# Kernel tuning notes

Hardware: AMD Instinct MI355X
Metric: run time of the kernel (lower is better)

The kernel has to match this reference:

```python
import jax, jax.numpy as jnp
import numpy as np
import math

N_COARSE, N_FINE = 8192, 32768
DEC_DIM, ENC_DIM, OUT_DIM, K = 256, 128, 128, 16
LN_EPS = 1e-5


def setup_inputs() -> dict:
    key = jax.random.key(0)
    ks = jax.random.split(key, 16)
    s = lambda fan_in: 1.0 / math.sqrt(fan_in)
    return {
        "decoder_features": jax.random.normal(ks[0], (N_COARSE, DEC_DIM), jnp.float32),
        "decoder_pos": jax.random.normal(ks[1], (N_COARSE, 3), jnp.float32),
        "encoder_features": jax.random.normal(ks[2], (N_FINE, ENC_DIM), jnp.float32),
        "encoder_pos": jax.random.normal(ks[3], (N_FINE, 3), jnp.float32),
        "encoder_labels": jax.random.randint(ks[4], (N_FINE,), 0, 13, jnp.int64),
        # params (torch nn.Linear default init scale)
        "Wq": jax.random.uniform(ks[5], (DEC_DIM, ENC_DIM), jnp.float32, -s(ENC_DIM), s(ENC_DIM)),
        "bq": jnp.zeros((DEC_DIM,), jnp.float32),
        "Wk": jax.random.uniform(ks[6], (DEC_DIM, DEC_DIM), jnp.float32, -s(DEC_DIM), s(DEC_DIM)),
        "bk": jnp.zeros((DEC_DIM,), jnp.float32),
        "Wv": jax.random.uniform(ks[7], (DEC_DIM, DEC_DIM), jnp.float32, -s(DEC_DIM), s(DEC_DIM)),
        "bv": jnp.zeros((DEC_DIM,), jnp.float32),
        "W1": jax.random.uniform(ks[8], (OUT_DIM, DEC_DIM + ENC_DIM), jnp.float32, -s(DEC_DIM + ENC_DIM), s(DEC_DIM + ENC_DIM)),
        "b1": jnp.zeros((OUT_DIM,), jnp.float32),
        "W2": jax.random.uniform(ks[9], (OUT_DIM, OUT_DIM), jnp.float32, -s(OUT_DIM), s(OUT_DIM)),
        "b2": jnp.zeros((OUT_DIM,), jnp.float32),
        "ln_g": jnp.ones((OUT_DIM,), jnp.float32),
        "ln_b": jnp.zeros((OUT_DIM,), jnp.float32),
    }


def _knn_indices(encoder_pos, decoder_pos, k):
    # For each fine (encoder) point, k nearest coarse (decoder) points.
    # squared distances [N_fine, N_coarse]
    d2 = (
        jnp.sum(encoder_pos * encoder_pos, axis=1, keepdims=True)
        - 2.0 * encoder_pos @ decoder_pos.T
        + jnp.sum(decoder_pos * decoder_pos, axis=1)[None, :]
    )
    _, idx = jax.lax.top_k(-d2, k)  # [N_fine, K]
    return idx


def reference(decoder_features, decoder_pos, encoder_features, encoder_pos,
              encoder_labels, Wq, bq, Wk, bk, Wv, bv, W1, b1, W2, b2, ln_g, ln_b):
    idx = _knn_indices(encoder_pos, decoder_pos, K)            # [Nf, K]
    nbr = decoder_features[idx]                                 # [Nf, K, Dd]
    query = encoder_features @ Wq.T + bq                        # [Nf, Dd]
    keys = nbr @ Wk.T + bk                                      # [Nf, K, Dd]
    values = nbr @ Wv.T + bv                                    # [Nf, K, Dd]
    scores = jnp.einsum('nd,nkd->nk', query, keys) / math.sqrt(DEC_DIM)
    # segment softmax over edges grouped by fine target == softmax over K
    weights = jax.nn.softmax(scores, axis=-1)                   # [Nf, K]
    agg = jnp.einsum('nk,nkd->nd', weights, values)             # [Nf, Dd]
    combined = jnp.concatenate([agg, encoder_features], axis=-1)
    h = jax.nn.relu(combined @ W1.T + b1)
    up = h @ W2.T + b2                                          # [Nf, out]
    mu = jnp.mean(up, axis=-1, keepdims=True)
    var = jnp.var(up, axis=-1, keepdims=True)
    out = (up - mu) * jax.lax.rsqrt(var + LN_EPS) * ln_g + ln_b
    # dropout is identity in eval mode
    return (out, encoder_pos, encoder_labels)
```

## Files before the change

### kernel.cpp

```cpp
#include <hip/hip_runtime.h>
#include <hip/hip_bf16.h>

typedef __hip_bfloat16 bf16;
typedef unsigned short u16;
typedef float f32x2 __attribute__((ext_vector_type(2)));

#define NC 8192
#define NF 32768
#define KNN 16
#define FMAXV 3.402823466e+38f

__device__ __forceinline__ float bfbits2f(u16 u){
  union { unsigned u; float f; } x; x.u = ((unsigned)u) << 16; return x.f;
}
__device__ __forceinline__ float asfloat(unsigned u){
  union { unsigned u; float f; } x; x.u = u; return x.f;
}
__device__ __forceinline__ f32x2 pk_fma(f32x2 a, f32x2 b, f32x2 c){
  f32x2 d;
  asm("v_pk_fma_f32 %0, %1, %2, %3" : "=v"(d) : "v"(a), "v"(b), "v"(c));
  return d;
}

__global__ __launch_bounds__(256) void k_pw(const float* __restrict__ dpos,
                                            const float* __restrict__ W1,
                                            const float* __restrict__ W2,
                                            float4* __restrict__ posP,
                                            float4* __restrict__ W1eSa,
                                            float4* __restrict__ W1eSb,
                                            float4* __restrict__ W2Sa,
                                            float4* __restrict__ W2Sb,
                                            const float* __restrict__ Wk,
                                            const float* __restrict__ Wv,
                                            const float* __restrict__ Wq,
                                            const float* __restrict__ bk,
                                            const float* __restrict__ bv,
                                            const float* __restrict__ bq,
                                            float* __restrict__ WkqS,
                                            float* __restrict__ WvuS,
                                            float* __restrict__ bkq,
                                            float* __restrict__ bvu,
                                            float* __restrict__ wbq,
                                            float* __restrict__ sbq){
  __shared__ float partial[256];
  __shared__ float red[256];
  int gb = blockIdx.x, t = threadIdx.x;
  if (gb >= 1028){
    int g = (gb - 1028) * 256 + t;
    if (g < 4096){
      const float2* dp2 = (const float2*)(dpos + (size_t)g * 6);
      float2 a = dp2[0], b = dp2[1], c = dp2[2];
      float x0 = a.x, y0 = a.y, z0 = b.x;
      float x1 = b.y, y1 = c.x, z1 = c.y;
      float dd0 = __fadd_rn(__fadd_rn(__fmul_rn(x0,x0), __fmul_rn(y0,y0)), __fmul_rn(z0,z0));
      float dd1 = __fadd_rn(__fadd_rn(__fmul_rn(x1,x1), __fmul_rn(y1,y1)), __fmul_rn(z1,z1));
      posP[g * 2]     = make_float4(x0, x1, y0, y1);
      posP[g * 2 + 1] = make_float4(z0, z1, dd0 * 0.5f, dd1 * 0.5f);
    } else if (g >= 8192 && g < 10240){
      int f = g - 8192; int c4 = f >> 6, jg = f & 63;
      W1eSa[f] = ((const float4*)(W1 + (size_t)(2 * jg) * 384 + 256))[c4];
    } else if (g >= 10240 && g < 12288){
      int f = g - 10240; int c4 = f >> 6, jg = f & 63;
      W1eSb[f] = ((const float4*)(W1 + (size_t)(2 * jg + 1) * 384 + 256))[c4];
    } else if (g >= 12288 && g < 14336){
      int f = g - 12288; int c4 = f >> 6, jg = f & 63;
      W2Sa[f] = ((const float4*)(W2 + (size_t)(2 * jg) * 128))[c4];
    } else if (g >= 14336 && g < 16384){
      int f = g - 14336; int c4 = f >> 6, jg = f & 63;
      W2Sb[f] = ((const float4*)(W2 + (size_t)(2 * jg + 1) * 128))[c4];
    }
    return;
  }
  int B = gb;
  int csel = B >> 2, tch = B & 3;
  int o = (t & 63) + tch * 64;
  int q = t >> 6;
  int j0 = q * 64;
  if (csel < 128){
    int c = csel;
    float acc = 0.f;
    for (int j = j0; j < j0 + 64; ++j)
      acc = fmaf(Wk[(size_t)j * 256 + o], Wq[(size_t)j * 128 + c], acc);
    partial[t] = acc;
    if (tch == 0) red[t] = bk[t] * Wq[(size_t)t * 128 + c];
    __syncthreads();
    if (t < 64){
      float a = partial[t] + partial[t + 64] + partial[t + 128] + partial[t + 192];
      WkqS[(size_t)((o >> 2) * 128 + c) * 4 + (o & 3)] = a;
    }
    if (tch == 0){
      for (int s = 128; s > 0; s >>= 1){ if (t < s) red[t] += red[t + s]; __syncthreads(); }
      if (t == 0) bkq[c] = red[0];
    }
  } else if (csel < 256){
    int h = csel - 128;
    float acc = 0.f;
    for (int j = j0; j < j0 + 64; ++j)
      acc = fmaf(Wv[(size_t)j * 256 + o], W1[(size_t)h * 384 + j], acc);
    partial[t] = acc;
    if (tch == 0) red[t] = bv[t] * W1[(size_t)h * 384 + t];
    __syncthreads();
    if (t < 64){
      float a = partial[t] + partial[t + 64] + partial[t + 128] + partial[t + 192];
      WvuS[(size_t)((o >> 2) * 128 + h) * 4 + (o & 3)] = a;
    }
    if (tch == 0){
      for (int s = 128; s > 0; s >>= 1){ if (t < s) red[t] += red[t + s]; __syncthreads(); }
      if (t == 0) bvu[h] = red[0];
    }
  } else {
    float acc = 0.f;
    for (int j = j0; j < j0 + 64; ++j)
      acc = fmaf(Wk[(size_t)j * 256 + o], bq[j], acc);
    partial[t] = acc;
    if (tch == 0) red[t] = bk[t] * bq[t];
    __syncthreads();
    if (t < 64){
      float a = partial[t] + partial[t + 64] + partial[t + 128] + partial[t + 192];
      wbq[o] = a;
    }
    if (tch == 0){
      for (int s = 128; s > 0; s >>= 1){ if (t < s) red[t] += red[t + s]; __syncthreads(); }
      if (t == 0) sbq[0] = red[0];
    }
  }
}

__global__ __launch_bounds__(256) void k_dk(const float* __restrict__ df,
                                            const float4* __restrict__ WkqS,
                                            const float4* __restrict__ WvuS,
                                            const float* __restrict__ bkq,
                                            const float* __restrict__ bvu,
                                            const float* __restrict__ wbq,
                                            const float* __restrict__ sbq,
                                            bf16* __restrict__ Zd, bf16* __restrict__ Ud,
                                            float* __restrict__ bqK,
                                            const float* __restrict__ epos,
                                            const float4* __restrict__ posP,
                                            int* __restrict__ knnI){
  __shared__ float dpart[8][32];
  __shared__ float smin[8 * 64];
  __shared__ float tauLDS[8];
  __shared__ int   cnt[8];
  __shared__ float lval[8][64];
  __shared__ int   lidx[8][64];

  int g = blockIdx.x, t = threadIdx.x;
  int m = g % 5, q5 = g / 5;
  if (m == 4){
    int g0 = q5 * 8;
    int half = __builtin_amdgcn_readfirstlane(t >> 7);
    int c = t & 127;
    const float4* W = half ? WvuS : WkqS;
    float acc[8];
    #pragma unroll
    for (int p = 0; p < 8; ++p) acc[p] = 0.f;
    for (int j4 = 0; j4 < 64; ++j4){
      float4 w = W[j4 * 128 + c];
      #pragma unroll
      for (int p = 0; p < 8; ++p){
        float4 a = ((const float4*)(df + (size_t)(g0 + p) * 256))[j4];
        acc[p] += w.x*a.x + w.y*a.y + w.z*a.z + w.w*a.w;
      }
    }
    float bias = half ? bvu[c] : bkq[c];
    bf16* dst = half ? Ud : Zd;
    #pragma unroll
    for (int p = 0; p < 8; ++p)
      dst[(size_t)(g0 + p) * 128 + c] = __float2bfloat16(acc[p] + bias);
    {
      int r = t >> 5, seg = t & 31;
      float s = 0.f;
      const float* dr = df + (size_t)(g0 + r) * 256 + seg * 8;
      const float* wq = wbq + seg * 8;
      #pragma unroll
      for (int e = 0; e < 8; ++e) s = fmaf(dr[e], wq[e], s);
      dpart[r][seg] = s;
    }
    __syncthreads();
    if (t < 8){
      float s = sbq[0];
      #pragma unroll
      for (int seg = 0; seg < 32; ++seg) s += dpart[t][seg];
      bqK[g0 + t] = s;
    }
    return;
  }

  int kb = q5 * 4 + m;
  int lane = t & 63, w = t >> 6;
  int n0 = kb * 8;
  f32x2 nex2[8], ney2[8], nez2[8];
  #pragma unroll
  for (int p = 0; p < 8; ++p){
    float nx = -epos[(n0 + p) * 3 + 0];
    float ny = -epos[(n0 + p) * 3 + 1];
    float nz = -epos[(n0 + p) * 3 + 2];
    nex2[p].x = nx; nex2[p].y = nx;
    ney2[p].x = ny; ney2[p].y = ny;
    nez2[p].x = nz; nez2[p].y = nz;
  }
  const float4* base = posP + w * 2048;

  f32x2 vmin2[8];
  #pragma unroll
  for (int p = 0; p < 8; ++p){ vmin2[p].x = FMAXV; vmin2[p].y = FMAXV; }
  #pragma unroll 4
  for (int s = 0; s < 16; ++s){
    int q2 = (s * 64 + lane) * 2;
    float4 XY = base[q2], ZW = base[q2 + 1];
    f32x2 X = {XY.x, XY.y}, Y = {XY.z, XY.w}, Z = {ZW.x, ZW.y}, W = {ZW.z, ZW.w};
    #pragma unroll
    for (int p = 0; p < 8; ++p){
      f32x2 v2 = pk_fma(nex2[p], X, W);
      v2 = pk_fma(ney2[p], Y, v2);
      v2 = pk_fma(nez2[p], Z, v2);
      vmin2[p].x = fminf(vmin2[p].x, v2.x);
      vmin2[p].y = fminf(vmin2[p].y, v2.y);
    }
  }
  float vmin[8];
  #pragma unroll
  for (int p = 0; p < 8; ++p) vmin[p] = fminf(vmin2[p].x, vmin2[p].y);

  #pragma unroll
  for (int k = 2; k <= 64; k <<= 1){
    #pragma unroll
    for (int j = k >> 1; j > 0; j >>= 1){
      bool keepmin = ((lane & j) == 0) == ((lane & k) == 0);
      #pragma unroll
      for (int p = 0; p < 8; ++p){
        float pv = __shfl_xor(vmin[p], j);
        vmin[p] = keepmin ? fminf(vmin[p], pv) : fmaxf(vmin[p], pv);
      }
    }
  }
  if (lane < 16){
    #pragma unroll
    for (int p = 0; p < 8; ++p) smin[p * 64 + w * 16 + lane] = vmin[p];
  }
  if (t < 8) cnt[t] = 0;
  __syncthreads();

  {
    int src = (lane & 16) ? (lane ^ 15) : lane;
    float v0 = smin[(w * 2 + 0) * 64 + src];
    float v1 = smin[(w * 2 + 1) * 64 + src];
    #pragma unroll
    for (int j = 16; j > 0; j >>= 1){
      bool keepmin = ((lane & 32) == 0) == ((lane & j) == 0);
      float p0 = __shfl_xor(v0, j); v0 = keepmin ? fminf(v0, p0) : fmaxf(v0, p0);
      float p1 = __shfl_xor(v1, j); v1 = keepmin ? fminf(v1, p1) : fmaxf(v1, p1);
    }
    #pragma unroll
    for (int j = 32; j > 0; j >>= 1){
      bool keepmin = ((lane & j) == 0);
      float p0 = __shfl_xor(v0, j); v0 = keepmin ? fminf(v0, p0) : fmaxf(v0, p0);
      float p1 = __shfl_xor(v1, j); v1 = keepmin ? fminf(v1, p1) : fmaxf(v1, p1);
    }
    if (lane == 16){ tauLDS[w * 2] = v0; tauLDS[w * 2 + 1] = v1; }
  }
  __syncthreads();
  float tau0[8];
  #pragma unroll
  for (int p = 0; p < 8; ++p) tau0[p] = tauLDS[p];

  #pragma unroll 2
  for (int s = 0; s < 16; ++s){
    int q = s * 64 + lane;
    float4 XY = base[q * 2], ZW = base[q * 2 + 1];
    f32x2 X = {XY.x, XY.y}, Y = {XY.z, XY.w}, Z = {ZW.x, ZW.y}, W = {ZW.z, ZW.w};
    int cand0 = w * 2048 + q * 2;
    #pragma unroll
    for (int p = 0; p < 8; ++p){
      f32x2 v2 = pk_fma(nex2[p], X, W);
      v2 = pk_fma(ney2[p], Y, v2);
      v2 = pk_fma(nez2[p], Z, v2);
      if (v2.x <= tau0[p]){
        int slot = atomicAdd(&cnt[p], 1);
        if (slot < 64){ lval[p][slot] = v2.x; lidx[p][slot] = cand0; }
      }
      if (v2.y <= tau0[p]){
        int slot = atomicAdd(&cnt[p], 1);
        if (slot < 64){ lval[p][slot] = v2.y; lidx[p][slot] = cand0 + 1; }
      }
    }
  }
  __syncthreads();

  {
    int p0 = w * 2, p1 = w * 2 + 1;
    int nA = n0 + p0, nB = n0 + p1;
    int c0 = cnt[p0]; if (c0 > 64) c0 = 64;
    int c1 = cnt[p1]; if (c1 > 64) c1 = 64;
    float va = (lane < c0) ? lval[p0][lane] : FMAXV;
    int   ia = (lane < c0) ? lidx[p0][lane] : 0x7fffffff;
    float vb = (lane < c1) ? lval[p1][lane] : FMAXV;
    int   ib = (lane < c1) ? lidx[p1][lane] : 0x7fffffff;

    #pragma unroll
    for (int k = 2; k <= 16; k <<= 1){
      #pragma unroll
      for (int j = k >> 1; j > 0; j >>= 1){
        bool keepmin = ((lane & k) == 0) == ((lane & j) == 0);
        { float pv = __shfl_xor(va, j); int pid = __shfl_xor(ia, j);
          bool pl = (pv < va) || (pv == va && pid < ia);
          if (keepmin ? pl : !pl){ va = pv; ia = pid; } }
        { float pv = __shfl_xor(vb, j); int pid = __shfl_xor(ib, j);
          bool pl = (pv < vb) || (pv == vb && pid < ib);
          if (keepmin ? pl : !pl){ vb = pv; ib = pid; } }
      }
    }
    { float pv = __shfl_xor(va, 16); int pid = __shfl_xor(ia, 16);
      if ((pv < va) || (pv == va && pid < ia)){ va = pv; ia = pid; } }
    { float pv = __shfl_xor(vb, 16); int pid = __shfl_xor(ib, 16);
      if ((pv < vb) || (pv == vb && pid < ib)){ vb = pv; ib = pid; } }
    #pragma unroll
    for (int j = 8; j > 0; j >>= 1){
      bool keepmin = ((lane & 32) == 0) == ((lane & j) == 0);
      { float pv = __shfl_xor(va, j); int pid = __shfl_xor(ia, j);
        bool pl = (pv < va) || (pv == va && pid < ia);
        if (keepmin ? pl : !pl){ va = pv; ia = pid; } }
      { float pv = __shfl_xor(vb, j); int pid = __shfl_xor(ib, j);
        bool pl = (pv < vb) || (pv == vb && pid < ib);
        if (keepmin ? pl : !pl){ vb = pv; ib = pid; } }
    }
    { float pv = __shfl_xor(va, 32); int pid = __shfl_xor(ia, 32);
      if ((pv < va) || (pv == va && pid < ia)){ va = pv; ia = pid; } }
    { float pv = __shfl_xor(vb, 32); int pid = __shfl_xor(ib, 32);
      if ((pv < vb) || (pv == vb && pid < ib)){ vb = pv; ib = pid; } }

    if (lane < 16){
      knnI[(size_t)nA * 16 + lane] = ia;
      knnI[(size_t)nB * 16 + lane] = ib;
    }
  }
}

__global__ __launch_bounds__(256) void k_amlp(const int* __restrict__ knnI,
                                              const bf16* __restrict__ Zd,
                                              const bf16* __restrict__ Ud,
                                              const float* __restrict__ bqK,
                                              const float* __restrict__ ef,
                                              const float4* __restrict__ W1eSa,
                                              const float4* __restrict__ W1eSb,
                                              const float* __restrict__ b1,
                                              const float4* __restrict__ W2Sa,
                                              const float4* __restrict__ W2Sb,
                                              const float* __restrict__ b2,
                                              const float* __restrict__ lng, const float* __restrict__ lnb,
                                              const float* __restrict__ epos, const int* __restrict__ lab,
                                              float* __restrict__ out){
  __shared__ float haggL[16 * 128];
  __shared__ float hbuf[16 * 128];
  __shared__ float ubuf[16 * 128];
  __shared__ float stats[32];
  int t = threadIdx.x;
  int n0 = blockIdx.x * 16;
  int lane = t & 63, w = t >> 6;
  {
    int gid = blockIdx.x * 256 + t;
    if (gid < NF){
      float* op = out + (size_t)NF * 128;
      op[gid * 3 + 0] = epos[gid * 3 + 0];
      op[gid * 3 + 1] = epos[gid * 3 + 1];
      op[gid * 3 + 2] = epos[gid * 3 + 2];
      out[(size_t)NF * 128 + (size_t)NF * 3 + gid] = (float)lab[gid];
    }
  }

  {
    int kk = lane & 15;
    int pp = w * 4 + (lane >> 4);
    int n = n0 + pp;
    int ik = knnI[(size_t)n * 16 + kk];
    const uint4*  zr = (const uint4*)((const u16*)Zd + (size_t)ik * 128);
    const float4* e4 = (const float4*)(ef + (size_t)n * 128);
    float pr = 0.f;
    #pragma unroll
    for (int i = 0; i < 16; ++i){
      uint4 z = zr[i];
      float4 ea = e4[2 * i], eb = e4[2 * i + 1];
      pr = fmaf(ea.x, asfloat(z.x << 16), pr); pr = fmaf(ea.y, asfloat(z.x & 0xffff0000u), pr);
      pr = fmaf(ea.z, asfloat(z.y << 16), pr); pr = fmaf(ea.w, asfloat(z.y & 0xffff0000u), pr);
      pr = fmaf(eb.x, asfloat(z.z << 16), pr); pr = fmaf(eb.y, asfloat(z.z & 0xffff0000u), pr);
      pr = fmaf(eb.z, asfloat(z.w << 16), pr); pr = fmaf(eb.w, asfloat(z.w & 0xffff0000u), pr);
    }
    float sc = (pr + bqK[ik]) * (1.0f / 16.0f);
    float mx = sc;
    #pragma unroll
    for (int off = 1; off < 16; off <<= 1) mx = fmaxf(mx, __shfl_xor(mx, off));
    float e = __expf(sc - mx);
    float l = e;
    #pragma unroll
    for (int off = 1; off < 16; off <<= 1) l += __shfl_xor(l, off);
    float wgt = e / l;

    float acc8[8];
    #pragma unroll
    for (int j = 0; j < 8; ++j) acc8[j] = 0.f;
    int gbase = lane & 48;
    #pragma unroll
    for (int k2 = 0; k2 < 16; ++k2){
      int src = gbase | k2;
      float wk = __shfl(wgt, src);
      int ikk = __shfl(ik, src);
      uint4 uu = *(const uint4*)((const u16*)Ud + (size_t)ikk * 128 + kk * 8);
      acc8[0] = fmaf(wk, asfloat(uu.x << 16), acc8[0]);
      acc8[1] = fmaf(wk, asfloat(uu.x & 0xffff0000u), acc8[1]);
      acc8[2] = fmaf(wk, asfloat(uu.y << 16), acc8[2]);
      acc8[3] = fmaf(wk, asfloat(uu.y & 0xffff0000u), acc8[3]);
      acc8[4] = fmaf(wk, asfloat(uu.z << 16), acc8[4]);
      acc8[5] = fmaf(wk, asfloat(uu.z & 0xffff0000u), acc8[5]);
      acc8[6] = fmaf(wk, asfloat(uu.w << 16), acc8[6]);
      acc8[7] = fmaf(wk, asfloat(uu.w & 0xffff0000u), acc8[7]);
    }
    float4* hp = (float4*)&haggL[pp * 128 + kk * 8];
    hp[0] = make_float4(acc8[0], acc8[1], acc8[2], acc8[3]);
    hp[1] = make_float4(acc8[4], acc8[5], acc8[6], acc8[7]);
  }

  int jg = t & 63;
  int pg4 = __builtin_amdgcn_readfirstlane((t >> 6) * 4);
  int j0 = jg * 2;
  float acc[2][4];
  #pragma unroll
  for (int a = 0; a < 2; ++a)
    #pragma unroll
    for (int p = 0; p < 4; ++p) acc[a][p] = 0.f;
  for (int c4 = 0; c4 < 32; ++c4){
    float4 wa = W1eSa[c4 * 64 + jg];
    float4 wb = W1eSb[c4 * 64 + jg];
    #pragma unroll
    for (int p = 0; p < 4; ++p){
      float4 x = ((const float4*)(ef + (size_t)(n0 + pg4 + p) * 128))[c4];
      acc[0][p] += wa.x*x.x + wa.y*x.y + wa.z*x.z + wa.w*x.w;
      acc[1][p] += wb.x*x.x + wb.y*x.y + wb.z*x.z + wb.w*x.w;
    }
  }
  __syncthreads();
  float b1a = b1[j0], b1b = b1[j0 + 1];
  #pragma unroll
  for (int p = 0; p < 4; ++p){
    float2 hgv = *(const float2*)&haggL[(pg4 + p) * 128 + j0];
    hbuf[(pg4 + p) * 128 + j0]     = fmaxf(acc[0][p] + b1a + hgv.x, 0.f);
    hbuf[(pg4 + p) * 128 + j0 + 1] = fmaxf(acc[1][p] + b1b + hgv.y, 0.f);
  }
  __syncthreads();
  float acc2[2][4];
  #pragma unroll
  for (int a = 0; a < 2; ++a)
    #pragma unroll
    for (int p = 0; p < 4; ++p) acc2[a][p] = 0.f;
  const float4* hb4 = (const float4*)hbuf;
  for (int c4 = 0; c4 < 32; ++c4){
    float4 wa = W2Sa[c4 * 64 + jg];
    float4 wb = W2Sb[c4 * 64 + jg];
    #pragma unroll
    for (int p = 0; p < 4; ++p){
      float4 x = hb4[(pg4 + p) * 32 + c4];
      acc2[0][p] += wa.x*x.x + wa.y*x.y + wa.z*x.z + wa.w*x.w;
      acc2[1][p] += wb.x*x.x + wb.y*x.y + wb.z*x.z + wb.w*x.w;
    }
  }
  float b2a = b2[j0], b2b = b2[j0 + 1];
  float u[2][4];
  #pragma unroll
  for (int p = 0; p < 4; ++p){
    u[0][p] = acc2[0][p] + b2a;
    u[1][p] = acc2[1][p] + b2b;
    ubuf[(pg4 + p) * 128 + j0]     = u[0][p];
    ubuf[(pg4 + p) * 128 + j0 + 1] = u[1][p];
  }
  __syncthreads();
  {
    int p = t >> 4, qi = t & 15;
    const float* ub = &ubuf[p * 128 + qi * 8];
    float s = 0.f, s2 = 0.f;
    #pragma unroll
    for (int e2i = 0; e2i < 8; ++e2i){ float v = ub[e2i]; s += v; s2 += v * v; }
    #pragma unroll
    for (int off = 1; off < 16; off <<= 1){ s += __shfl_xor(s, off); s2 += __shfl_xor(s2, off); }
    if (qi == 0){
      float mu = s * (1.f / 128.f);
      float var = s2 * (1.f / 128.f) - mu * mu;
      stats[p] = mu;
      stats[16 + p] = rsqrtf(fmaxf(var, 0.f) + 1e-5f);
    }
  }
  __syncthreads();
  float ga = lng[j0], gb = lng[j0 + 1];
  float ba = lnb[j0], bbv = lnb[j0 + 1];
  #pragma unroll
  for (int p = 0; p < 4; ++p){
    float mu = stats[pg4 + p], rs = stats[16 + pg4 + p];
    out[(size_t)(n0 + pg4 + p) * 128 + j0]     = (u[0][p] - mu) * rs * ga + ba;
    out[(size_t)(n0 + pg4 + p) * 128 + j0 + 1] = (u[1][p] - mu) * rs * gb + bbv;
  }
}

extern "C" void kernel_launch(void* const* d_in, const int* in_sizes, int n_in,
                              void* d_out, int out_size, void* d_ws, size_t ws_size,
                              hipStream_t stream){
  const float* df   = (const float*)d_in[0];
  const float* dpos = (const float*)d_in[1];
  const float* ef   = (const float*)d_in[2];
  const float* epos = (const float*)d_in[3];
  const int*   lab  = (const int*)d_in[4];
  const float* Wq = (const float*)d_in[5];
  const float* bq = (const float*)d_in[6];
  const float* Wk = (const float*)d_in[7];
  const float* bk = (const float*)d_in[8];
  const float* Wv = (const float*)d_in[9];
  const float* bv = (const float*)d_in[10];
  const float* W1 = (const float*)d_in[11];
  const float* b1 = (const float*)d_in[12];
  const float* W2 = (const float*)d_in[13];
  const float* b2 = (const float*)d_in[14];
  const float* lng = (const float*)d_in[15];
  const float* lnb = (const float*)d_in[16];
  float* out = (float*)d_out;

  char* wsb = (char*)d_ws;
  float4* posP  = (float4*)(wsb);
  bf16*   Zd    = (bf16*)(wsb + 131072);
  bf16*   Ud    = (bf16*)(wsb + 2228224);
  float*  bqK   = (float*)(wsb + 4325376);
  int*    knnI  = (int*)(wsb + 4358144);
  float4* W1eSa = (float4*)(wsb + 12746752);
  float4* W1eSb = (float4*)(wsb + 12779520);
  float4* W2Sa  = (float4*)(wsb + 12812288);
  float4* W2Sb  = (float4*)(wsb + 12845056);
  float*  WkqS  = (float*)(wsb + 12877824);
  float*  WvuS  = (float*)(wsb + 13008896);
  float*  bkq   = (float*)(wsb + 13139968);
  float*  bvu   = (float*)(wsb + 13140480);
  float*  wbq   = (float*)(wsb + 13140992);
  float*  sbq   = (float*)(wsb + 13142016);

  k_pw   <<<1092, 256, 0, stream>>>(dpos, W1, W2, posP, W1eSa, W1eSb, W2Sa, W2Sb,
                                    Wk, Wv, Wq, bk, bv, bq, WkqS, WvuS, bkq, bvu, wbq, sbq);
  k_dk   <<<5120, 256, 0, stream>>>(df, (const float4*)WkqS, (const float4*)WvuS, bkq, bvu, wbq, sbq,
                                    Zd, Ud, bqK, epos, posP, knnI);
  k_amlp <<<NF / 16, 256, 0, stream>>>(knnI, Zd, Ud, bqK, ef, W1eSa, W1eSb, b1, W2Sa, W2Sb, b2, lng, lnb, epos, lab, out);
  (void)in_sizes; (void)n_in; (void)out_size; (void)ws_size;
}
```

Measured before the change: 333.5 us.

## Replace LDS atomics with wave ballot compaction, batch gathers, move passthrough copy

The candidate collection in the kNN pass now uses per-wave ballot/popcount prefix compaction into per-wave LDS lists instead of shared-memory atomicAdd. The lists are then merged by segment offsets. The attention/MLP kernel batches its Zd and Ud gather loads eight at a time to raise memory-level parallelism and adds unroll pragmas to the two dense loops. The position/label passthrough copy moves into extra blocks of the setup kernel. This trades more LDS and registers for fewer atomics and better latency hiding.

```diff
diff --git a/kernel.cpp b/kernel.cpp
--- a/kernel.cpp
+++ b/kernel.cpp
@@ -41,10 +41,24 @@
                                             float* __restrict__ bkq,
                                             float* __restrict__ bvu,
                                             float* __restrict__ wbq,
-                                            float* __restrict__ sbq){
+                                            float* __restrict__ sbq,
+                                            const float* __restrict__ epos,
+                                            const int* __restrict__ lab,
+                                            float* __restrict__ out){
   __shared__ float partial[256];
   __shared__ float red[256];
   int gb = blockIdx.x, t = threadIdx.x;
+  if (gb >= 1092){
+    int gid = (gb - 1092) * 256 + t;
+    if (gid < NF){
+      float* op = out + (size_t)NF * 128;
+      op[gid * 3 + 0] = epos[gid * 3 + 0];
+      op[gid * 3 + 1] = epos[gid * 3 + 1];
+      op[gid * 3 + 2] = epos[gid * 3 + 2];
+      out[(size_t)NF * 128 + (size_t)NF * 3 + gid] = (float)lab[gid];
+    }
+    return;
+  }
   if (gb >= 1028){
     int g = (gb - 1028) * 256 + t;
     if (g < 4096){
@@ -141,9 +155,9 @@
   __shared__ float dpart[8][32];
   __shared__ float smin[8 * 64];
   __shared__ float tauLDS[8];
-  __shared__ int   cnt[8];
-  __shared__ float lval[8][64];
-  __shared__ int   lidx[8][64];
+  __shared__ int   cntL[8][4];
+  __shared__ float lval[8][4][64];
+  __shared__ int   lidx[8][4][64];
 
   int g = blockIdx.x, t = threadIdx.x;
   int m = g % 5, q5 = g / 5;
@@ -239,7 +253,6 @@
     #pragma unroll
     for (int p = 0; p < 8; ++p) smin[p * 64 + w * 16 + lane] = vmin[p];
   }
-  if (t < 8) cnt[t] = 0;
   __syncthreads();
 
   {
@@ -265,6 +278,8 @@
   #pragma unroll
   for (int p = 0; p < 8; ++p) tau0[p] = tauLDS[p];
 
+  unsigned long long lmlt = (1ull << lane) - 1ull;
+  int cnt[8] = {0,0,0,0,0,0,0,0};
   #pragma unroll 2
   for (int s = 0; s < 16; ++s){
     int q = s * 64 + lane;
@@ -276,27 +291,46 @@
       f32x2 v2 = pk_fma(nex2[p], X, W);
       v2 = pk_fma(ney2[p], Y, v2);
       v2 = pk_fma(nez2[p], Z, v2);
-      if (v2.x <= tau0[p]){
-        int slot = atomicAdd(&cnt[p], 1);
-        if (slot < 64){ lval[p][slot] = v2.x; lidx[p][slot] = cand0; }
-      }
-      if (v2.y <= tau0[p]){
-        int slot = atomicAdd(&cnt[p], 1);
-        if (slot < 64){ lval[p][slot] = v2.y; lidx[p][slot] = cand0 + 1; }
-      }
-    }
+      bool h0 = v2.x <= tau0[p];
+      bool h1 = v2.y <= tau0[p];
+      unsigned long long m0 = __ballot(h0);
+      unsigned long long m1 = __ballot(h1);
+      if (m0 | m1){
+        int base0 = cnt[p];
+        int c0 = (int)__popcll(m0);
+        if (h0){
+          int s0 = base0 + (int)__popcll(m0 & lmlt);
+          if (s0 < 64){ lval[p][w][s0] = v2.x; lidx[p][w][s0] = cand0; }
+        }
+        if (h1){
+          int s1 = base0 + c0 + (int)__popcll(m1 & lmlt);
+          if (s1 < 64){ lval[p][w][s1] = v2.y; lidx[p][w][s1] = cand0 + 1; }
+        }
+        cnt[p] = base0 + c0 + (int)__popcll(m1);
+      }
+    }
+  }
+  if (lane == 0){
+    #pragma unroll
+    for (int p = 0; p < 8; ++p) cntL[p][w] = (cnt[p] > 64) ? 64 : cnt[p];
   }
   __syncthreads();
 
   {
     int p0 = w * 2, p1 = w * 2 + 1;
     int nA = n0 + p0, nB = n0 + p1;
-    int c0 = cnt[p0]; if (c0 > 64) c0 = 64;
-    int c1 = cnt[p1]; if (c1 > 64) c1 = 64;
-    float va = (lane < c0) ? lval[p0][lane] : FMAXV;
-    int   ia = (lane < c0) ? lidx[p0][lane] : 0x7fffffff;
-    float vb = (lane < c1) ? lval[p1][lane] : FMAXV;
-    int   ib = (lane < c1) ? lidx[p1][lane] : 0x7fffffff;
+    int cA0 = cntL[p0][0], cA1 = cntL[p0][1], cA2 = cntL[p0][2], cA3 = cntL[p0][3];
+    int cB0 = cntL[p1][0], cB1 = cntL[p1][1], cB2 = cntL[p1][2], cB3 = cntL[p1][3];
+    int oA1 = cA0, oA2 = oA1 + cA1, oA3 = oA2 + cA2; int totA = oA3 + cA3; if (totA > 64) totA = 64;
+    int oB1 = cB0, oB2 = oB1 + cB1, oB3 = oB2 + cB2; int totB = oB3 + cB3; if (totB > 64) totB = 64;
+    int segA = (lane >= oA1) + (lane >= oA2) + (lane >= oA3);
+    int segB = (lane >= oB1) + (lane >= oB2) + (lane >= oB3);
+    int basA = segA == 0 ? 0 : (segA == 1 ? oA1 : (segA == 2 ? oA2 : oA3));
+    int basB = segB == 0 ? 0 : (segB == 1 ? oB1 : (segB == 2 ? oB2 : oB3));
+    float va = (lane < totA) ? lval[p0][segA][lane - basA] : FMAXV;
+    int   ia = (lane < totA) ? lidx[p0][segA][lane - basA] : 0x7fffffff;
+    float vb = (lane < totB) ? lval[p1][segB][lane - basB] : FMAXV;
+    int   ib = (lane < totB) ? lidx[p1][segB][lane - basB] : 0x7fffffff;
 
     #pragma unroll
     for (int k = 2; k <= 16; k <<= 1){
@@ -349,7 +383,6 @@
                                               const float4* __restrict__ W2Sb,
                                               const float* __restrict__ b2,
                                               const float* __restrict__ lng, const float* __restrict__ lnb,
-                                              const float* __restrict__ epos, const int* __restrict__ lab,
                                               float* __restrict__ out){
   __shared__ float haggL[16 * 128];
   __shared__ float hbuf[16 * 128];
@@ -358,35 +391,42 @@
   int t = threadIdx.x;
   int n0 = blockIdx.x * 16;
   int lane = t & 63, w = t >> 6;
-  {
-    int gid = blockIdx.x * 256 + t;
-    if (gid < NF){
-      float* op = out + (size_t)NF * 128;
-      op[gid * 3 + 0] = epos[gid * 3 + 0];
-      op[gid * 3 + 1] = epos[gid * 3 + 1];
-      op[gid * 3 + 2] = epos[gid * 3 + 2];
-      out[(size_t)NF * 128 + (size_t)NF * 3 + gid] = (float)lab[gid];
-    }
-  }
 
   {
     int kk = lane & 15;
     int pp = w * 4 + (lane >> 4);
     int n = n0 + pp;
     int ik = knnI[(size_t)n * 16 + kk];
+    float bz = bqK[ik];
     const uint4*  zr = (const uint4*)((const u16*)Zd + (size_t)ik * 128);
     const float4* e4 = (const float4*)(ef + (size_t)n * 128);
     float pr = 0.f;
-    #pragma unroll
-    for (int i = 0; i < 16; ++i){
-      uint4 z = zr[i];
-      float4 ea = e4[2 * i], eb = e4[2 * i + 1];
-      pr = fmaf(ea.x, asfloat(z.x << 16), pr); pr = fmaf(ea.y, asfloat(z.x & 0xffff0000u), pr);
-      pr = fmaf(ea.z, asfloat(z.y << 16), pr); pr = fmaf(ea.w, asfloat(z.y & 0xffff0000u), pr);
-      pr = fmaf(eb.x, asfloat(z.z << 16), pr); pr = fmaf(eb.y, asfloat(z.z & 0xffff0000u), pr);
-      pr = fmaf(eb.z, asfloat(z.w << 16), pr); pr = fmaf(eb.w, asfloat(z.w & 0xffff0000u), pr);
-    }
-    float sc = (pr + bqK[ik]) * (1.0f / 16.0f);
+    {
+      uint4 zb[8];
+      #pragma unroll
+      for (int i = 0; i < 8; ++i) zb[i] = zr[i];
+      #pragma unroll
+      for (int i = 0; i < 8; ++i){
+        uint4 z = zb[i];
+        float4 ea = e4[2 * i], eb = e4[2 * i + 1];
+        pr = fmaf(ea.x, asfloat(z.x << 16), pr); pr = fmaf(ea.y, asfloat(z.x & 0xffff0000u), pr);
+        pr = fmaf(ea.z, asfloat(z.y << 16), pr); pr = fmaf(ea.w, asfloat(z.y & 0xffff0000u), pr);
+        pr = fmaf(eb.x, asfloat(z.z << 16), pr); pr = fmaf(eb.y, asfloat(z.z & 0xffff0000u), pr);
+        pr = fmaf(eb.z, asfloat(z.w << 16), pr); pr = fmaf(eb.w, asfloat(z.w & 0xffff0000u), pr);
+      }
+      #pragma unroll
+      for (int i = 0; i < 8; ++i) zb[i] = zr[8 + i];
+      #pragma unroll
+      for (int i = 0; i < 8; ++i){
+        uint4 z = zb[i];
+        float4 ea = e4[2 * (8 + i)], eb = e4[2 * (8 + i) + 1];
+        pr = fmaf(ea.x, asfloat(z.x << 16), pr); pr = fmaf(ea.y, asfloat(z.x & 0xffff0000u), pr);
+        pr = fmaf(ea.z, asfloat(z.y << 16), pr); pr = fmaf(ea.w, asfloat(z.y & 0xffff0000u), pr);
+        pr = fmaf(eb.x, asfloat(z.z << 16), pr); pr = fmaf(eb.y, asfloat(z.z & 0xffff0000u), pr);
+        pr = fmaf(eb.z, asfloat(z.w << 16), pr); pr = fmaf(eb.w, asfloat(z.w & 0xffff0000u), pr);
+      }
+    }
+    float sc = (pr + bz) * (1.0f / 16.0f);
     float mx = sc;
     #pragma unroll
     for (int off = 1; off < 16; off <<= 1) mx = fmaxf(mx, __shfl_xor(mx, off));
@@ -396,24 +436,46 @@
     for (int off = 1; off < 16; off <<= 1) l += __shfl_xor(l, off);
     float wgt = e / l;
 
+    int gbase = lane & 48;
+    float wk[16]; int ikk[16];
+    #pragma unroll
+    for (int k2 = 0; k2 < 16; ++k2){
+      wk[k2]  = __shfl(wgt, gbase | k2);
+      ikk[k2] = __shfl(ik,  gbase | k2);
+    }
     float acc8[8];
     #pragma unroll
     for (int j = 0; j < 8; ++j) acc8[j] = 0.f;
-    int gbase = lane & 48;
-    #pragma unroll
-    for (int k2 = 0; k2 < 16; ++k2){
-      int src = gbase | k2;
-      float wk = __shfl(wgt, src);
-      int ikk = __shfl(ik, src);
-      uint4 uu = *(const uint4*)((const u16*)Ud + (size_t)ikk * 128 + kk * 8);
-      acc8[0] = fmaf(wk, asfloat(uu.x << 16), acc8[0]);
-      acc8[1] = fmaf(wk, asfloat(uu.x & 0xffff0000u), acc8[1]);
-      acc8[2] = fmaf(wk, asfloat(uu.y << 16), acc8[2]);
-      acc8[3] = fmaf(wk, asfloat(uu.y & 0xffff0000u), acc8[3]);
-      acc8[4] = fmaf(wk, asfloat(uu.z << 16), acc8[4]);
-      acc8[5] = fmaf(wk, asfloat(uu.z & 0xffff0000u), acc8[5]);
-      acc8[6] = fmaf(wk, asfloat(uu.w << 16), acc8[6]);
-      acc8[7] = fmaf(wk, asfloat(uu.w & 0xffff0000u), acc8[7]);
+    {
+      uint4 ub[8];
+      #pragma unroll
+      for (int k2 = 0; k2 < 8; ++k2) ub[k2] = *(const uint4*)((const u16*)Ud + (size_t)ikk[k2] * 128 + kk * 8);
+      #pragma unroll
+      for (int k2 = 0; k2 < 8; ++k2){
+        uint4 uu = ub[k2]; float wv = wk[k2];
+        acc8[0] = fmaf(wv, asfloat(uu.x << 16), acc8[0]);
+        acc8[1] = fmaf(wv, asfloat(uu.x & 0xffff0000u), acc8[1]);
+        acc8[2] = fmaf(wv, asfloat(uu.y << 16), acc8[2]);
+        acc8[3] = fmaf(wv, asfloat(uu.y & 0xffff0000u), acc8[3]);
+        acc8[4] = fmaf(wv, asfloat(uu.z << 16), acc8[4]);
+        acc8[5] = fmaf(wv, asfloat(uu.z & 0xffff0000u), acc8[5]);
+        acc8[6] = fmaf(wv, asfloat(uu.w << 16), acc8[6]);
+        acc8[7] = fmaf(wv, asfloat(uu.w & 0xffff0000u), acc8[7]);
+      }
+      #pragma unroll
+      for (int k2 = 0; k2 < 8; ++k2) ub[k2] = *(const uint4*)((const u16*)Ud + (size_t)ikk[8 + k2] * 128 + kk * 8);
+      #pragma unroll
+      for (int k2 = 0; k2 < 8; ++k2){
+        uint4 uu = ub[k2]; float wv = wk[8 + k2];
+        acc8[0] = fmaf(wv, asfloat(uu.x << 16), acc8[0]);
+        acc8[1] = fmaf(wv, asfloat(uu.x & 0xffff0000u), acc8[1]);
+        acc8[2] = fmaf(wv, asfloat(uu.y << 16), acc8[2]);
+        acc8[3] = fmaf(wv, asfloat(uu.y & 0xffff0000u), acc8[3]);
+        acc8[4] = fmaf(wv, asfloat(uu.z << 16), acc8[4]);
+        acc8[5] = fmaf(wv, asfloat(uu.z & 0xffff0000u), acc8[5]);
+        acc8[6] = fmaf(wv, asfloat(uu.w << 16), acc8[6]);
+        acc8[7] = fmaf(wv, asfloat(uu.w & 0xffff0000u), acc8[7]);
+      }
     }
     float4* hp = (float4*)&haggL[pp * 128 + kk * 8];
     hp[0] = make_float4(acc8[0], acc8[1], acc8[2], acc8[3]);
@@ -428,6 +490,7 @@
   for (int a = 0; a < 2; ++a)
     #pragma unroll
     for (int p = 0; p < 4; ++p) acc[a][p] = 0.f;
+  #pragma unroll 4
   for (int c4 = 0; c4 < 32; ++c4){
     float4 wa = W1eSa[c4 * 64 + jg];
     float4 wb = W1eSb[c4 * 64 + jg];
@@ -453,6 +516,7 @@
     #pragma unroll
     for (int p = 0; p < 4; ++p) acc2[a][p] = 0.f;
   const float4* hb4 = (const float4*)hbuf;
+  #pragma unroll 4
   for (int c4 = 0; c4 < 32; ++c4){
     float4 wa = W2Sa[c4 * 64 + jg];
     float4 wb = W2Sb[c4 * 64 + jg];
@@ -538,10 +602,11 @@
   float*  wbq   = (float*)(wsb + 13140992);
   float*  sbq   = (float*)(wsb + 13142016);
 
-  k_pw   <<<1092, 256, 0, stream>>>(dpos, W1, W2, posP, W1eSa, W1eSb, W2Sa, W2Sb,
-                                    Wk, Wv, Wq, bk, bv, bq, WkqS, WvuS, bkq, bvu, wbq, sbq);
+  k_pw   <<<1220, 256, 0, stream>>>(dpos, W1, W2, posP, W1eSa, W1eSb, W2Sa, W2Sb,
+                                    Wk, Wv, Wq, bk, bv, bq, WkqS, WvuS, bkq, bvu, wbq, sbq,
+                                    epos, lab, out);
   k_dk   <<<5120, 256, 0, stream>>>(df, (const float4*)WkqS, (const float4*)WvuS, bkq, bvu, wbq, sbq,
                                     Zd, Ud, bqK, epos, posP, knnI);
-  k_amlp <<<NF / 16, 256, 0, stream>>>(knnI, Zd, Ud, bqK, ef, W1eSa, W1eSb, b1, W2Sa, W2Sb, b2, lng, lnb, epos, lab, out);
+  k_amlp <<<NF / 16, 256, 0, stream>>>(knnI, Zd, Ud, bqK, ef, W1eSa, W1eSb, b1, W2Sa, W2Sb, b2, lng, lnb, out);
   (void)in_sizes; (void)n_in; (void)out_size; (void)ws_size;
 }
```

After: 320.0 us. 1.04x faster.
